# Kernel tuning notes

Measured on AMD Instinct MI355X. Metric: run time of the kernel, lower is better.

Reference implementation:

```python
import jax, jax.numpy as jnp
import numpy as np

N_NODES = 100000
N_EDGES = 1600000
NIN = 128
NHID = 128
N_GRAPHS = 1024


def _gcn_conv(x, src, dst, norm, W, b, n_nodes):
    """PyG-style GCNConv: linear (no bias) -> normalized scatter-add -> + bias."""
    xw = x @ W                                   # [N, out]
    msg = xw[src] * norm[:, None]                # gather + edge-normalize, [E', out]
    out = jax.ops.segment_sum(msg, dst, num_segments=n_nodes)
    return out + b


def _gcn_norm(edge_index, n_nodes):
    """Add self-loops and compute symmetric deg^{-1/2} normalization per edge."""
    loops = jnp.arange(n_nodes, dtype=edge_index.dtype)
    src = jnp.concatenate([edge_index[0], loops])
    dst = jnp.concatenate([edge_index[1], loops])
    deg = jax.ops.segment_sum(jnp.ones_like(dst, dtype=jnp.float32), dst,
                              num_segments=n_nodes)
    deg_isqrt = jnp.where(deg > 0, jax.lax.rsqrt(jnp.maximum(deg, 1.0)), 0.0)
    norm = deg_isqrt[src] * deg_isqrt[dst]
    return src, dst, norm


def setup_inputs() -> dict:
    key = jax.random.key(0)
    ks = jax.random.split(key, 8)
    x = jax.random.normal(ks[0], (N_NODES, NIN), dtype=jnp.float32)
    edge_index = jax.random.randint(ks[1], (2, N_EDGES), 0, N_NODES, dtype=jnp.int64)
    batch = jnp.sort(jax.random.randint(ks[2], (N_NODES,), 0, N_GRAPHS, dtype=jnp.int64))
    s_in = 1.0 / np.sqrt(NIN)
    s_h = 1.0 / np.sqrt(NHID)
    return {
        "x": x,
        "edge_index": edge_index,
        "batch": batch,
        "W1": jax.random.normal(ks[3], (NIN, NHID), dtype=jnp.float32) * s_in,
        "b1": jnp.zeros((NHID,), dtype=jnp.float32),
        "W2": jax.random.normal(ks[4], (NHID, NHID), dtype=jnp.float32) * s_h,
        "b2": jnp.zeros((NHID,), dtype=jnp.float32),
        "W3": jax.random.normal(ks[5], (NHID, NHID), dtype=jnp.float32) * s_h,
        "b3": jnp.zeros((NHID,), dtype=jnp.float32),
        "Wfc": jax.random.normal(ks[6], (NHID, 1), dtype=jnp.float32) * s_h,
        "bfc": jnp.zeros((1,), dtype=jnp.float32),
    }


def reference(x, edge_index, batch, W1, b1, W2, b2, W3, b3, Wfc, bfc):
    n_nodes = x.shape[0]
    src, dst, norm = _gcn_norm(edge_index, n_nodes)
    h = jax.nn.relu(_gcn_conv(x, src, dst, norm, W1, b1, n_nodes))
    h = jax.nn.relu(_gcn_conv(h, src, dst, norm, W2, b2, n_nodes))
    h = jax.nn.relu(_gcn_conv(h, src, dst, norm, W3, b3, n_nodes))
    # global mean pool over graphs in the batch
    sums = jax.ops.segment_sum(h, batch, num_segments=N_GRAPHS)      # [G, NHID]
    cnts = jax.ops.segment_sum(jnp.ones((n_nodes,), dtype=h.dtype), batch,
                               num_segments=N_GRAPHS)
    pooled = sums / jnp.maximum(cnts, 1.0)[:, None]
    return pooled @ Wfc + bfc                                        # [G, 1]
```

## Files before the change

### kernel.cpp

```cpp
#include <hip/hip_runtime.h>

#define N_NODES   100000
#define N_EDGES   1600000
#define NFEAT     128
#define N_GRAPHS  1024

#define BSHIFT  8
#define BNODES  256
#define NBUCK   391
#define BCAP    4608
#define SC_EDGES 4096
#define SC_EPT   8
#define SC_BLOCKS 391
#define BD_EPT   18

#define WT_STRIDE 136
#define GEMM_BLOCKS 782

typedef unsigned int uint32;
typedef unsigned short ushort;
typedef __attribute__((ext_vector_type(8))) short short8;
typedef __attribute__((ext_vector_type(4))) float f32x4;

__device__ inline ushort f2b(float f) {
    uint32 x = __float_as_uint(f);
    uint32 r = x + 0x7fffu + ((x >> 16) & 1u);
    return (ushort)(r >> 16);
}
__device__ inline float blo(uint32 u) { return __uint_as_float(u << 16); }
__device__ inline float bhi(uint32 u) { return __uint_as_float(u & 0xffff0000u); }

__device__ inline short8 cvt8(const float* p) {
    float4 v0 = ((const float4*)p)[0];
    float4 v1 = ((const float4*)p)[1];
    short8 r;
    r[0] = (short)f2b(v0.x); r[1] = (short)f2b(v0.y);
    r[2] = (short)f2b(v0.z); r[3] = (short)f2b(v0.w);
    r[4] = (short)f2b(v1.x); r[5] = (short)f2b(v1.y);
    r[6] = (short)f2b(v1.z); r[7] = (short)f2b(v1.w);
    return r;
}

__global__ __launch_bounds__(256) void k_castw(const float* __restrict__ W1, const float* __restrict__ W2,
                                               const float* __restrict__ W3, ushort* __restrict__ WT,
                                               int* __restrict__ cur) {
    int i = blockIdx.x * blockDim.x + threadIdx.x;
    if (i < NBUCK) cur[i] = 0;
    if (i >= 3 * NFEAT * NFEAT) return;
    int l = i >> 14;
    int j = i & 16383;
    int n = j >> 7;
    int k = j & 127;
    const float* W = (l == 0) ? W1 : (l == 1) ? W2 : W3;
    WT[i] = f2b(W[k * NFEAT + n]);
}

struct SMemScatter {
    int hist[NBUCK], lofs[NBUCK], gbase[NBUCK];
    int wsum[4];
    uint32 sortedP[SC_EDGES];
    ushort sortedB[SC_EDGES];
};

__global__ __launch_bounds__(512) void k_phase1(const int* __restrict__ src, const int* __restrict__ dst,
                                                int* __restrict__ cur, uint32* __restrict__ bbuf,
                                                const float* __restrict__ A, const ushort* __restrict__ WTl,
                                                ushort* __restrict__ C, int M) {
    __shared__ __align__(16) char smem[NFEAT * WT_STRIDE * 2];
    int t = threadIdx.x;
    if (blockIdx.x < SC_BLOCKS) {
        SMemScatter& S = *(SMemScatter*)smem;
        int e0 = blockIdx.x * SC_EDGES;
        int total = N_EDGES - e0; if (total > SC_EDGES) total = SC_EDGES; if (total < 0) total = 0;
        for (int i = t; i < NBUCK; i += 512) S.hist[i] = 0;
        __syncthreads();
        uint32 val[SC_EPT];
        int    meta[SC_EPT];
        #pragma unroll
        for (int k = 0; k < SC_EPT; ++k) {
            int i = t + k * 512;
            meta[k] = -1;
            if (i < total) {
                int s = src[e0 + i], d = dst[e0 + i];
                int b = d >> BSHIFT;
                int tk = atomicAdd(&S.hist[b], 1);
                val[k] = ((uint32)(d & (BNODES - 1)) << 17) | (uint32)s;
                meta[k] = (b << 13) | tk;
            }
        }
        __syncthreads();
        int inc = 0, ts = 0, h0 = 0;
        if (t < 256) {
            int b0 = 2 * t, b1 = 2 * t + 1;
            h0 = (b0 < NBUCK) ? S.hist[b0] : 0;
            int h1 = (b1 < NBUCK) ? S.hist[b1] : 0;
            ts = h0 + h1;
            int lane = t & 63;
            inc = ts;
            #pragma unroll
            for (int d = 1; d < 64; d <<= 1) {
                int u = __shfl_up(inc, d, 64);
                if (lane >= d) inc += u;
            }
            if (lane == 63) S.wsum[t >> 6] = inc;
        }
        __syncthreads();
        if (t < 256) {
            int w = t >> 6;
            int wpre = 0;
            for (int i = 0; i < w; ++i) wpre += S.wsum[i];
            int run = wpre + inc - ts;
            int b0 = 2 * t, b1 = 2 * t + 1;
            int h1 = ts - h0;
            if (b0 < NBUCK) {
                S.lofs[b0] = run;
                if (h0) S.gbase[b0] = atomicAdd(&cur[b0], h0);
            }
            if (b1 < NBUCK) {
                S.lofs[b1] = run + h0;
                if (h1) S.gbase[b1] = atomicAdd(&cur[b1], h1);
            }
        }
        __syncthreads();
        #pragma unroll
        for (int k = 0; k < SC_EPT; ++k) {
            if (meta[k] >= 0) {
                int b = meta[k] >> 13;
                int p = S.lofs[b] + (meta[k] & 0x1FFF);
                S.sortedP[p] = val[k];
                S.sortedB[p] = (ushort)b;
            }
        }
        __syncthreads();
        for (int i = t; i < total; i += 512) {
            int b = S.sortedB[i];
            int addr = S.gbase[b] + (i - S.lofs[b]);
            if (addr < BCAP)
                bbuf[(size_t)b * BCAP + addr] = S.sortedP[i];
        }
    } else {
        ushort* sWT = (ushort*)smem;
        int gb = blockIdx.x - SC_BLOCKS;
        for (int i = t; i < NFEAT * 16; i += 512) {
            int n = i >> 4, c = i & 15;
            *(float4*)(sWT + n * WT_STRIDE + c * 8) = ((const float4*)WTl)[i];
        }
        int wave = t >> 6, lane = t & 63;
        int m0 = gb * 128 + wave * 16;
        int mRow = m0 + (lane & 15);
        if (mRow >= M) mRow = M - 1;
        int kg = lane >> 4;
        const float* Ap = A + (size_t)mRow * NFEAT + kg * 8;
        short8 a0 = cvt8(Ap);
        short8 a1 = cvt8(Ap + 32);
        short8 a2 = cvt8(Ap + 64);
        short8 a3 = cvt8(Ap + 96);
        __syncthreads();

        f32x4 acc[8];
        #pragma unroll
        for (int nt = 0; nt < 8; ++nt) acc[nt] = (f32x4){0.f, 0.f, 0.f, 0.f};
        #pragma unroll
        for (int nt = 0; nt < 8; ++nt) {
            int n = nt * 16 + (lane & 15);
            const short8* Bp = (const short8*)(sWT + n * WT_STRIDE + kg * 8);
            short8 b0 = Bp[0];
            short8 b1 = Bp[4];
            short8 b2 = Bp[8];
            short8 b3 = Bp[12];
            acc[nt] = __builtin_amdgcn_mfma_f32_16x16x32_bf16(a0, b0, acc[nt], 0, 0, 0);
            acc[nt] = __builtin_amdgcn_mfma_f32_16x16x32_bf16(a1, b1, acc[nt], 0, 0, 0);
            acc[nt] = __builtin_amdgcn_mfma_f32_16x16x32_bf16(a2, b2, acc[nt], 0, 0, 0);
            acc[nt] = __builtin_amdgcn_mfma_f32_16x16x32_bf16(a3, b3, acc[nt], 0, 0, 0);
        }
        __syncthreads();
        {
            int colBase = lane & 15;
            #pragma unroll
            for (int r = 0; r < 4; ++r) {
                int lr = wave * 16 + kg * 4 + r;
                #pragma unroll
                for (int nt = 0; nt < 8; ++nt)
                    sWT[lr * NFEAT + nt * 16 + colBase] = f2b(acc[nt][r]);
            }
        }
        __syncthreads();
        {
            int rowBase = gb * 128;
            const float4* sC4 = (const float4*)sWT;
            for (int i = t; i < 2048; i += 512) {
                int row = i >> 4;
                int gr = rowBase + row;
                if (gr < M) ((float4*)(C + (size_t)gr * NFEAT))[i & 15] = sC4[i];
            }
        }
    }
}

__global__ __launch_bounds__(256) void k_build(const uint32* __restrict__ bbuf, const int* __restrict__ cur,
                                               int* __restrict__ col, int* __restrict__ offsets,
                                               float* __restrict__ dinv) {
    int b = blockIdx.x;
    __shared__ int hist[BNODES], excl[BNODES];
    __shared__ int wsum[4], wtot[4];
    __shared__ int sorted[BCAP];
    __shared__ int sBase, sTotal;
    int t = threadIdx.x;
    {
        int pre = 0, tot = 0;
        #pragma unroll
        for (int q = 0; q < 2; ++q) {
            int i = 2 * t + q;
            if (i < NBUCK) {
                int v = cur[i]; if (v > BCAP) v = BCAP;
                tot += v;
                if (i < b) pre += v;
            }
        }
        int lane = t & 63, w = t >> 6;
        #pragma unroll
        for (int d = 32; d > 0; d >>= 1) { pre += __shfl_down(pre, d, 64); tot += __shfl_down(tot, d, 64); }
        if (lane == 0) { wsum[w] = pre; wtot[w] = tot; }
        __syncthreads();
        if (t == 0) {
            sBase = wsum[0] + wsum[1] + wsum[2] + wsum[3];
            sTotal = wtot[0] + wtot[1] + wtot[2] + wtot[3];
        }
        hist[t] = 0;
    }
    __syncthreads();
    int base = sBase;
    if (b == NBUCK - 1 && t == 0) offsets[N_NODES] = sTotal;
    int cnt = cur[b]; if (cnt > BCAP) cnt = BCAP;
    const uint32* reg = bbuf + (size_t)b * BCAP;

    uint32 val[BD_EPT];
    int    meta[BD_EPT];
    #pragma unroll
    for (int k = 0; k < BD_EPT; ++k) {
        int i = t + k * 256;
        meta[k] = -1;
        if (i < cnt) {
            uint32 p = reg[i];
            int node = p >> 17;
            int tk = atomicAdd(&hist[node], 1);
            val[k] = p & 0x1FFFF;
            meta[k] = (node << 16) | tk;
        }
    }
    __syncthreads();
    {
        int c = hist[t];
        int lane = t & 63, w = t >> 6;
        int inc = c;
        #pragma unroll
        for (int d = 1; d < 64; d <<= 1) {
            int u = __shfl_up(inc, d, 64);
            if (lane >= d) inc += u;
        }
        if (lane == 63) wsum[w] = inc;
        __syncthreads();
        int wpre = 0;
        for (int i = 0; i < w; ++i) wpre += wsum[i];
        int e = wpre + inc - c;
        excl[t] = e;
        int node = (b << BSHIFT) + t;
        if (node < N_NODES) {
            offsets[node] = base + e;
            dinv[node] = rsqrtf((float)(c + 1));
        }
    }
    __syncthreads();
    #pragma unroll
    for (int k = 0; k < BD_EPT; ++k) {
        if (meta[k] >= 0) {
            int node = meta[k] >> 16;
            sorted[excl[node] + (meta[k] & 0xFFFF)] = (int)val[k];
        }
    }
    __syncthreads();
    for (int i = t; i < cnt; i += 256) col[base + i] = sorted[i];
}

__global__ __launch_bounds__(512) void k_gemm(const ushort* __restrict__ A,
                                              const ushort* __restrict__ WTl,
                                              ushort* __restrict__ C, int M) {
    __shared__ ushort sWT[NFEAT * WT_STRIDE];
    int t = threadIdx.x;
    for (int i = t; i < NFEAT * 16; i += 512) {
        int n = i >> 4, c = i & 15;
        *(float4*)(sWT + n * WT_STRIDE + c * 8) = ((const float4*)WTl)[i];
    }
    int wave = t >> 6, lane = t & 63;
    int m0 = blockIdx.x * 128 + wave * 16;
    int mRow = m0 + (lane & 15);
    if (mRow >= M) mRow = M - 1;
    int kg = lane >> 4;
    const short8* Ap = (const short8*)(A + (size_t)mRow * NFEAT + kg * 8);
    short8 a0 = Ap[0];
    short8 a1 = Ap[4];
    short8 a2 = Ap[8];
    short8 a3 = Ap[12];
    __syncthreads();

    f32x4 acc[8];
    #pragma unroll
    for (int nt = 0; nt < 8; ++nt) acc[nt] = (f32x4){0.f, 0.f, 0.f, 0.f};
    #pragma unroll
    for (int nt = 0; nt < 8; ++nt) {
        int n = nt * 16 + (lane & 15);
        const short8* Bp = (const short8*)(sWT + n * WT_STRIDE + kg * 8);
        short8 b0 = Bp[0];
        short8 b1 = Bp[4];
        short8 b2 = Bp[8];
        short8 b3 = Bp[12];
        acc[nt] = __builtin_amdgcn_mfma_f32_16x16x32_bf16(a0, b0, acc[nt], 0, 0, 0);
        acc[nt] = __builtin_amdgcn_mfma_f32_16x16x32_bf16(a1, b1, acc[nt], 0, 0, 0);
        acc[nt] = __builtin_amdgcn_mfma_f32_16x16x32_bf16(a2, b2, acc[nt], 0, 0, 0);
        acc[nt] = __builtin_amdgcn_mfma_f32_16x16x32_bf16(a3, b3, acc[nt], 0, 0, 0);
    }
    __syncthreads();
    {
        int colBase = lane & 15;
        #pragma unroll
        for (int r = 0; r < 4; ++r) {
            int lr = wave * 16 + kg * 4 + r;
            #pragma unroll
            for (int nt = 0; nt < 8; ++nt)
                sWT[lr * NFEAT + nt * 16 + colBase] = f2b(acc[nt][r]);
        }
    }
    __syncthreads();
    {
        int rowBase = blockIdx.x * 128;
        const float4* sC4 = (const float4*)sWT;
        for (int i = t; i < 2048; i += 512) {
            int row = i >> 4;
            int gr = rowBase + row;
            if (gr < M) ((float4*)(C + (size_t)gr * NFEAT))[i & 15] = sC4[i];
        }
    }
}

#define AGG_BODY4 \
    float dn = dinv[n]; \
    int half = lane >> 4; \
    int fl = lane & 15; \
    const uint4* XW4 = (const uint4*)XWu; \
    uint4 sv = XW4[(size_t)n * 16 + fl]; \
    float ws = (half == 0) ? dn * dn : 0.f; \
    float a0 = ws * blo(sv.x), a1 = ws * bhi(sv.x); \
    float a2 = ws * blo(sv.y), a3 = ws * bhi(sv.y); \
    float a4 = ws * blo(sv.z), a5 = ws * bhi(sv.z); \
    float a6 = ws * blo(sv.w), a7 = ws * bhi(sv.w); \
    int e0 = off[n], e1 = off[n + 1]; \
    for (int base = e0; base < e1; base += 64) { \
        int len = e1 - base; if (len > 64) len = 64; \
        int cm = (lane < len) ? col[base + lane] : 0; \
        float wm = (lane < len) ? dn * dinv[cm] : 0.f; \
        int j = 0; \
        for (; j + 16 <= len; j += 16) { \
            uint4 u[4]; float w[4]; \
            _Pragma("unroll") \
            for (int p = 0; p < 4; ++p) { \
                int idx = j + 4 * p + half; \
                int cc = __shfl(cm, idx, 64); \
                w[p] = __shfl(wm, idx, 64); \
                u[p] = XW4[(size_t)cc * 16 + fl]; \
            } \
            _Pragma("unroll") \
            for (int p = 0; p < 4; ++p) { \
                a0 = fmaf(w[p], blo(u[p].x), a0); a1 = fmaf(w[p], bhi(u[p].x), a1); \
                a2 = fmaf(w[p], blo(u[p].y), a2); a3 = fmaf(w[p], bhi(u[p].y), a3); \
                a4 = fmaf(w[p], blo(u[p].z), a4); a5 = fmaf(w[p], bhi(u[p].z), a5); \
                a6 = fmaf(w[p], blo(u[p].w), a6); a7 = fmaf(w[p], bhi(u[p].w), a7); \
            } \
        } \
        for (; j < len; j += 4) { \
            int rem = len - j; \
            int idx = j + ((half < rem) ? half : 0); \
            int cc = __shfl(cm, idx, 64); \
            float ww = __shfl(wm, idx, 64); \
            if (half >= rem) ww = 0.f; \
            uint4 u = XW4[(size_t)cc * 16 + fl]; \
            a0 = fmaf(ww, blo(u.x), a0); a1 = fmaf(ww, bhi(u.x), a1); \
            a2 = fmaf(ww, blo(u.y), a2); a3 = fmaf(ww, bhi(u.y), a3); \
            a4 = fmaf(ww, blo(u.z), a4); a5 = fmaf(ww, bhi(u.z), a5); \
            a6 = fmaf(ww, blo(u.w), a6); a7 = fmaf(ww, bhi(u.w), a7); \
        } \
    } \
    a0 += __shfl_xor(a0, 32, 64); a0 += __shfl_xor(a0, 16, 64); \
    a1 += __shfl_xor(a1, 32, 64); a1 += __shfl_xor(a1, 16, 64); \
    a2 += __shfl_xor(a2, 32, 64); a2 += __shfl_xor(a2, 16, 64); \
    a3 += __shfl_xor(a3, 32, 64); a3 += __shfl_xor(a3, 16, 64); \
    a4 += __shfl_xor(a4, 32, 64); a4 += __shfl_xor(a4, 16, 64); \
    a5 += __shfl_xor(a5, 32, 64); a5 += __shfl_xor(a5, 16, 64); \
    a6 += __shfl_xor(a6, 32, 64); a6 += __shfl_xor(a6, 16, 64); \
    a7 += __shfl_xor(a7, 32, 64); a7 += __shfl_xor(a7, 16, 64);

__global__ __launch_bounds__(256) void k_agg(const uint32* __restrict__ XWu, const int* __restrict__ col,
                                             const int* __restrict__ off, const float* __restrict__ dinv,
                                             const float* __restrict__ bias, uint32* __restrict__ Hu) {
    int wid = (blockIdx.x * blockDim.x + threadIdx.x) >> 6;
    int lane = threadIdx.x & 63;
    if (wid >= N_NODES) return;
    int n = wid;
    AGG_BODY4
    if (half == 0) {
        float4 bb0 = ((const float4*)bias)[2 * fl];
        float4 bb1 = ((const float4*)bias)[2 * fl + 1];
        float r0 = fmaxf(a0 + bb0.x, 0.f), r1 = fmaxf(a1 + bb0.y, 0.f);
        float r2 = fmaxf(a2 + bb0.z, 0.f), r3 = fmaxf(a3 + bb0.w, 0.f);
        float r4 = fmaxf(a4 + bb1.x, 0.f), r5 = fmaxf(a5 + bb1.y, 0.f);
        float r6 = fmaxf(a6 + bb1.z, 0.f), r7 = fmaxf(a7 + bb1.w, 0.f);
        uint4 o;
        o.x = (uint32)f2b(r0) | ((uint32)f2b(r1) << 16);
        o.y = (uint32)f2b(r2) | ((uint32)f2b(r3) << 16);
        o.z = (uint32)f2b(r4) | ((uint32)f2b(r5) << 16);
        o.w = (uint32)f2b(r6) | ((uint32)f2b(r7) << 16);
        ((uint4*)Hu)[(size_t)n * 16 + fl] = o;
    }
}

__global__ __launch_bounds__(256) void k_agg_fc(const uint32* __restrict__ XWu, const int* __restrict__ col,
                                                const int* __restrict__ off, const float* __restrict__ dinv,
                                                const float* __restrict__ bias, const float* __restrict__ Wfc,
                                                float* __restrict__ nodeS) {
    int wid = (blockIdx.x * blockDim.x + threadIdx.x) >> 6;
    int lane = threadIdx.x & 63;
    if (wid >= N_NODES) return;
    int n = wid;
    AGG_BODY4
    float4 bb0 = ((const float4*)bias)[2 * fl];
    float4 bb1 = ((const float4*)bias)[2 * fl + 1];
    float4 wf0 = ((const float4*)Wfc)[2 * fl];
    float4 wf1 = ((const float4*)Wfc)[2 * fl + 1];
    float s = fmaxf(a0 + bb0.x, 0.f) * wf0.x + fmaxf(a1 + bb0.y, 0.f) * wf0.y
            + fmaxf(a2 + bb0.z, 0.f) * wf0.z + fmaxf(a3 + bb0.w, 0.f) * wf0.w
            + fmaxf(a4 + bb1.x, 0.f) * wf1.x + fmaxf(a5 + bb1.y, 0.f) * wf1.y
            + fmaxf(a6 + bb1.z, 0.f) * wf1.z + fmaxf(a7 + bb1.w, 0.f) * wf1.w;
    s += __shfl_xor(s, 8, 64);
    s += __shfl_xor(s, 4, 64);
    s += __shfl_xor(s, 2, 64);
    s += __shfl_xor(s, 1, 64);
    if (lane == 0) nodeS[n] = s;
}

__device__ inline int lower_bound_dev(const int* a, int n, int key) {
    int lo = 0, hi = n;
    while (lo < hi) {
        int mid = (lo + hi) >> 1;
        if (a[mid] < key) lo = mid + 1; else hi = mid;
    }
    return lo;
}

__global__ __launch_bounds__(256) void k_pool(const float* __restrict__ nodeS, const int* __restrict__ batch,
                                              const float* __restrict__ bfc, float* __restrict__ out) {
    int g = blockIdx.x;
    int t = threadIdx.x;
    int lo = lower_bound_dev(batch, N_NODES, g);
    int hi = lower_bound_dev(batch, N_NODES, g + 1);
    float s = 0.f;
    for (int i = lo + t; i < hi; i += 256) s += nodeS[i];
    for (int d = 32; d > 0; d >>= 1) s += __shfl_down(s, d, 64);
    __shared__ float ws[4];
    int lane = t & 63, w = t >> 6;
    if (lane == 0) ws[w] = s;
    __syncthreads();
    if (t == 0) {
        float tot = ws[0] + ws[1] + ws[2] + ws[3];
        float cnt = (float)(hi - lo);
        out[g] = tot / fmaxf(cnt, 1.0f) + bfc[0];
    }
}

extern "C" void kernel_launch(void* const* d_in, const int* in_sizes, int n_in,
                              void* d_out, int out_size, void* d_ws, size_t ws_size,
                              hipStream_t stream) {
    const float* x    = (const float*)d_in[0];
    const int*   ei   = (const int*)d_in[1];
    const int*   batch= (const int*)d_in[2];
    const float* W1   = (const float*)d_in[3];
    const float* b1   = (const float*)d_in[4];
    const float* W2   = (const float*)d_in[5];
    const float* b2   = (const float*)d_in[6];
    const float* W3   = (const float*)d_in[7];
    const float* b3   = (const float*)d_in[8];
    const float* Wfc  = (const float*)d_in[9];
    const float* bfc  = (const float*)d_in[10];
    float* out = (float*)d_out;

    const int* src = ei;
    const int* dst = ei + N_EDGES;

    char* p = (char*)d_ws;
    auto carve = [&](size_t bytes) { void* r = (void*)p; p += (bytes + 255) & ~(size_t)255; return r; };
    int*    cur       = (int*)   carve(sizeof(int) * NBUCK);
    uint32* bbuf      = (uint32*)carve(sizeof(uint32) * (size_t)NBUCK * BCAP);
    float*  dinv      = (float*) carve(sizeof(float) * N_NODES);
    int*    offsets   = (int*)   carve(sizeof(int) * (N_NODES + 1));
    int*    col       = (int*)   carve(sizeof(int) * N_EDGES);
    ushort* XW        = (ushort*)carve(sizeof(short) * (size_t)N_NODES * NFEAT);
    ushort* H         = (ushort*)carve(sizeof(short) * (size_t)N_NODES * NFEAT);
    ushort* WT        = (ushort*)carve(sizeof(short) * 3 * NFEAT * NFEAT);
    float*  nodeS     = (float*) carve(sizeof(float) * N_NODES);

    const int waveNodeBlocks = (N_NODES * 64 + 255) / 256;

    k_castw<<<(3 * NFEAT * NFEAT + 255) / 256, 256, 0, stream>>>(W1, W2, W3, WT, cur);
    k_phase1<<<SC_BLOCKS + GEMM_BLOCKS, 512, 0, stream>>>(src, dst, cur, bbuf, x, WT, XW, N_NODES);
    k_build<<<NBUCK, 256, 0, stream>>>(bbuf, cur, col, offsets, dinv);

    k_agg<<<waveNodeBlocks, 256, 0, stream>>>((const uint32*)XW, col, offsets, dinv, b1, (uint32*)H);
    k_gemm<<<GEMM_BLOCKS, 512, 0, stream>>>(H, WT + NFEAT * NFEAT, XW, N_NODES);
    k_agg<<<waveNodeBlocks, 256, 0, stream>>>((const uint32*)XW, col, offsets, dinv, b2, (uint32*)H);
    k_gemm<<<GEMM_BLOCKS, 512, 0, stream>>>(H, WT + 2 * NFEAT * NFEAT, XW, N_NODES);
    k_agg_fc<<<waveNodeBlocks, 256, 0, stream>>>((const uint32*)XW, col, offsets, dinv, b3, Wfc, nodeS);

    k_pool<<<N_GRAPHS, 256, 0, stream>>>(nodeS, batch, bfc, out);
}
```

Measured before the change: 372.5 us.

## Split first-layer GEMM across scatter and CSR-build kernels, drop weight cast kernel

Removes the standalone weight-cast kernel: W1 is converted and transposed straight into shared memory inside the GEMM body, and the W2/W3 casts run as extra blocks in phase 1. The first-layer X·W1 GEMM is split in half, one half co-scheduled with the edge scatter and the other half with the CSR build, which now uses 512 threads. The goal is to fill the GPU during the latency-bound graph-preprocessing kernels and cut one launch. The trade-off is that every GEMM block recasts W1 from fp32 with scattered 2-byte LDS writes, and the counter reset becomes a memset.

New measurement: 378.4 us. Within noise of the previous version (+1.6%).

```diff
diff --git a/kernel.cpp b/kernel.cpp
--- a/kernel.cpp
+++ b/kernel.cpp
@@ -12,10 +12,12 @@
 #define SC_EDGES 4096
 #define SC_EPT   8
 #define SC_BLOCKS 391
-#define BD_EPT   18
+#define CW_BLOCKS 64
+#define BD_EPT   9
 
 #define WT_STRIDE 136
 #define GEMM_BLOCKS 782
+#define GEMM_SPLIT  391
 
 typedef unsigned int uint32;
 typedef unsigned short ushort;
@@ -41,18 +43,67 @@
     return r;
 }
 
-__global__ __launch_bounds__(256) void k_castw(const float* __restrict__ W1, const float* __restrict__ W2,
-                                               const float* __restrict__ W3, ushort* __restrict__ WT,
-                                               int* __restrict__ cur) {
-    int i = blockIdx.x * blockDim.x + threadIdx.x;
-    if (i < NBUCK) cur[i] = 0;
-    if (i >= 3 * NFEAT * NFEAT) return;
-    int l = i >> 14;
-    int j = i & 16383;
-    int n = j >> 7;
-    int k = j & 127;
-    const float* W = (l == 0) ? W1 : (l == 1) ? W2 : W3;
-    WT[i] = f2b(W[k * NFEAT + n]);
+__device__ __forceinline__ void gemm_x_body(ushort* sWT, int t, int gb,
+                                            const float* __restrict__ A,
+                                            const float* __restrict__ W1,
+                                            ushort* __restrict__ C, int M) {
+    for (int i = t; i < NFEAT * 32; i += 512) {
+        int k = i >> 5, n0 = (i & 31) * 4;
+        float4 v = ((const float4*)W1)[i];
+        sWT[(n0 + 0) * WT_STRIDE + k] = f2b(v.x);
+        sWT[(n0 + 1) * WT_STRIDE + k] = f2b(v.y);
+        sWT[(n0 + 2) * WT_STRIDE + k] = f2b(v.z);
+        sWT[(n0 + 3) * WT_STRIDE + k] = f2b(v.w);
+    }
+    int wave = t >> 6, lane = t & 63;
+    int m0 = gb * 128 + wave * 16;
+    int mRow = m0 + (lane & 15);
+    if (mRow >= M) mRow = M - 1;
+    int kg = lane >> 4;
+    const float* Ap = A + (size_t)mRow * NFEAT + kg * 8;
+    short8 a0 = cvt8(Ap);
+    short8 a1 = cvt8(Ap + 32);
+    short8 a2 = cvt8(Ap + 64);
+    short8 a3 = cvt8(Ap + 96);
+    __syncthreads();
+
+    f32x4 acc[8];
+    #pragma unroll
+    for (int nt = 0; nt < 8; ++nt) acc[nt] = (f32x4){0.f, 0.f, 0.f, 0.f};
+    #pragma unroll
+    for (int nt = 0; nt < 8; ++nt) {
+        int n = nt * 16 + (lane & 15);
+        const short8* Bp = (const short8*)(sWT + n * WT_STRIDE + kg * 8);
+        short8 b0 = Bp[0];
+        short8 b1 = Bp[4];
+        short8 b2 = Bp[8];
+        short8 b3 = Bp[12];
+        acc[nt] = __builtin_amdgcn_mfma_f32_16x16x32_bf16(a0, b0, acc[nt], 0, 0, 0);
+        acc[nt] = __builtin_amdgcn_mfma_f32_16x16x32_bf16(a1, b1, acc[nt], 0, 0, 0);
+        acc[nt] = __builtin_amdgcn_mfma_f32_16x16x32_bf16(a2, b2, acc[nt], 0, 0, 0);
+        acc[nt] = __builtin_amdgcn_mfma_f32_16x16x32_bf16(a3, b3, acc[nt], 0, 0, 0);
+    }
+    __syncthreads();
+    {
+        int colBase = lane & 15;
+        #pragma unroll
+        for (int r = 0; r < 4; ++r) {
+            int lr = wave * 16 + kg * 4 + r;
+            #pragma unroll
+            for (int nt = 0; nt < 8; ++nt)
+                sWT[lr * NFEAT + nt * 16 + colBase] = f2b(acc[nt][r]);
+        }
+    }
+    __syncthreads();
+    {
+        int rowBase = gb * 128;
+        const float4* sC4 = (const float4*)sWT;
+        for (int i = t; i < 2048; i += 512) {
+            int row = i >> 4;
+            int gr = rowBase + row;
+            if (gr < M) ((float4*)(C + (size_t)gr * NFEAT))[i & 15] = sC4[i];
+        }
+    }
 }
 
 struct SMemScatter {
@@ -64,8 +115,9 @@
 
 __global__ __launch_bounds__(512) void k_phase1(const int* __restrict__ src, const int* __restrict__ dst,
                                                 int* __restrict__ cur, uint32* __restrict__ bbuf,
-                                                const float* __restrict__ A, const ushort* __restrict__ WTl,
-                                                ushort* __restrict__ C, int M) {
+                                                const float* __restrict__ A, const float* __restrict__ W1,
+                                                const float* __restrict__ W2, const float* __restrict__ W3,
+                                                ushort* __restrict__ WT, ushort* __restrict__ C, int M) {
     __shared__ __align__(16) char smem[NFEAT * WT_STRIDE * 2];
     int t = threadIdx.x;
     if (blockIdx.x < SC_BLOCKS) {
@@ -138,148 +190,114 @@
             if (addr < BCAP)
                 bbuf[(size_t)b * BCAP + addr] = S.sortedP[i];
         }
+    } else if (blockIdx.x < SC_BLOCKS + CW_BLOCKS) {
+        int i = (blockIdx.x - SC_BLOCKS) * 512 + t;
+        int l = i >> 14;
+        int j = i & 16383;
+        int n = j >> 7;
+        int k = j & 127;
+        const float* W = l ? W3 : W2;
+        WT[i] = f2b(W[k * NFEAT + n]);
     } else {
-        ushort* sWT = (ushort*)smem;
-        int gb = blockIdx.x - SC_BLOCKS;
-        for (int i = t; i < NFEAT * 16; i += 512) {
-            int n = i >> 4, c = i & 15;
-            *(float4*)(sWT + n * WT_STRIDE + c * 8) = ((const float4*)WTl)[i];
-        }
-        int wave = t >> 6, lane = t & 63;
-        int m0 = gb * 128 + wave * 16;
-        int mRow = m0 + (lane & 15);
-        if (mRow >= M) mRow = M - 1;
-        int kg = lane >> 4;
-        const float* Ap = A + (size_t)mRow * NFEAT + kg * 8;
-        short8 a0 = cvt8(Ap);
-        short8 a1 = cvt8(Ap + 32);
-        short8 a2 = cvt8(Ap + 64);
-        short8 a3 = cvt8(Ap + 96);
-        __syncthreads();
-
-        f32x4 acc[8];
+        int gb = blockIdx.x - (SC_BLOCKS + CW_BLOCKS);
+        gemm_x_body((ushort*)smem, t, gb, A, W1, C, M);
+    }
+}
+
+__global__ __launch_bounds__(512) void k_phase2(const uint32* __restrict__ bbuf, const int* __restrict__ cur,
+                                                int* __restrict__ col, int* __restrict__ offsets,
+                                                float* __restrict__ dinv,
+                                                const float* __restrict__ A, const float* __restrict__ W1,
+                                                ushort* __restrict__ C, int M) {
+    __shared__ __align__(16) char smem[NFEAT * WT_STRIDE * 2];
+    int t = threadIdx.x;
+    if (blockIdx.x < NBUCK) {
+        struct SB {
+            int hist[BNODES], excl[BNODES];
+            int wsum[8], wtot[8];
+            int sorted[BCAP];
+            int sBase, sTotal;
+        };
+        SB& S = *(SB*)smem;
+        int b = blockIdx.x;
+        {
+            int v = 0;
+            if (t < NBUCK) { v = cur[t]; if (v > BCAP) v = BCAP; }
+            int pre = (t < b) ? v : 0;
+            int tot = v;
+            int lane = t & 63, w = t >> 6;
+            #pragma unroll
+            for (int d = 32; d > 0; d >>= 1) { pre += __shfl_down(pre, d, 64); tot += __shfl_down(tot, d, 64); }
+            if (lane == 0) { S.wsum[w] = pre; S.wtot[w] = tot; }
+            if (t < BNODES) S.hist[t] = 0;
+        }
+        __syncthreads();
+        if (t == 0) {
+            int pb = 0, tb2 = 0;
+            #pragma unroll
+            for (int i = 0; i < 8; ++i) { pb += S.wsum[i]; tb2 += S.wtot[i]; }
+            S.sBase = pb; S.sTotal = tb2;
+        }
+        __syncthreads();
+        int base = S.sBase;
+        if (b == NBUCK - 1 && t == 0) offsets[N_NODES] = S.sTotal;
+        int cnt = cur[b]; if (cnt > BCAP) cnt = BCAP;
+        const uint32* reg = bbuf + (size_t)b * BCAP;
+
+        uint32 val[BD_EPT];
+        int    meta[BD_EPT];
         #pragma unroll
-        for (int nt = 0; nt < 8; ++nt) acc[nt] = (f32x4){0.f, 0.f, 0.f, 0.f};
+        for (int k = 0; k < BD_EPT; ++k) {
+            int i = t + k * 512;
+            meta[k] = -1;
+            if (i < cnt) {
+                uint32 p = reg[i];
+                int node = p >> 17;
+                int tk = atomicAdd(&S.hist[node], 1);
+                val[k] = p & 0x1FFFF;
+                meta[k] = (node << 16) | tk;
+            }
+        }
+        __syncthreads();
+        int c = 0, inc = 0;
+        if (t < 256) {
+            c = S.hist[t];
+            int lane = t & 63;
+            inc = c;
+            #pragma unroll
+            for (int d = 1; d < 64; d <<= 1) {
+                int u = __shfl_up(inc, d, 64);
+                if (lane >= d) inc += u;
+            }
+            if (lane == 63) S.wsum[t >> 6] = inc;
+        }
+        __syncthreads();
+        if (t < 256) {
+            int w = t >> 6;
+            int wpre = 0;
+            for (int i = 0; i < w; ++i) wpre += S.wsum[i];
+            int e = wpre + inc - c;
+            S.excl[t] = e;
+            int node = (b << BSHIFT) + t;
+            if (node < N_NODES) {
+                offsets[node] = base + e;
+                dinv[node] = rsqrtf((float)(c + 1));
+            }
+        }
+        __syncthreads();
         #pragma unroll
-        for (int nt = 0; nt < 8; ++nt) {
-            int n = nt * 16 + (lane & 15);
-            const short8* Bp = (const short8*)(sWT + n * WT_STRIDE + kg * 8);
-            short8 b0 = Bp[0];
-            short8 b1 = Bp[4];
-            short8 b2 = Bp[8];
-            short8 b3 = Bp[12];
-            acc[nt] = __builtin_amdgcn_mfma_f32_16x16x32_bf16(a0, b0, acc[nt], 0, 0, 0);
-            acc[nt] = __builtin_amdgcn_mfma_f32_16x16x32_bf16(a1, b1, acc[nt], 0, 0, 0);
-            acc[nt] = __builtin_amdgcn_mfma_f32_16x16x32_bf16(a2, b2, acc[nt], 0, 0, 0);
-            acc[nt] = __builtin_amdgcn_mfma_f32_16x16x32_bf16(a3, b3, acc[nt], 0, 0, 0);
-        }
-        __syncthreads();
-        {
-            int colBase = lane & 15;
-            #pragma unroll
-            for (int r = 0; r < 4; ++r) {
-                int lr = wave * 16 + kg * 4 + r;
-                #pragma unroll
-                for (int nt = 0; nt < 8; ++nt)
-                    sWT[lr * NFEAT + nt * 16 + colBase] = f2b(acc[nt][r]);
-            }
-        }
-        __syncthreads();
-        {
-            int rowBase = gb * 128;
-            const float4* sC4 = (const float4*)sWT;
-            for (int i = t; i < 2048; i += 512) {
-                int row = i >> 4;
-                int gr = rowBase + row;
-                if (gr < M) ((float4*)(C + (size_t)gr * NFEAT))[i & 15] = sC4[i];
-            }
-        }
-    }
-}
-
-__global__ __launch_bounds__(256) void k_build(const uint32* __restrict__ bbuf, const int* __restrict__ cur,
-                                               int* __restrict__ col, int* __restrict__ offsets,
-                                               float* __restrict__ dinv) {
-    int b = blockIdx.x;
-    __shared__ int hist[BNODES], excl[BNODES];
-    __shared__ int wsum[4], wtot[4];
-    __shared__ int sorted[BCAP];
-    __shared__ int sBase, sTotal;
-    int t = threadIdx.x;
-    {
-        int pre = 0, tot = 0;
-        #pragma unroll
-        for (int q = 0; q < 2; ++q) {
-            int i = 2 * t + q;
-            if (i < NBUCK) {
-                int v = cur[i]; if (v > BCAP) v = BCAP;
-                tot += v;
-                if (i < b) pre += v;
-            }
-        }
-        int lane = t & 63, w = t >> 6;
-        #pragma unroll
-        for (int d = 32; d > 0; d >>= 1) { pre += __shfl_down(pre, d, 64); tot += __shfl_down(tot, d, 64); }
-        if (lane == 0) { wsum[w] = pre; wtot[w] = tot; }
-        __syncthreads();
-        if (t == 0) {
-            sBase = wsum[0] + wsum[1] + wsum[2] + wsum[3];
-            sTotal = wtot[0] + wtot[1] + wtot[2] + wtot[3];
-        }
-        hist[t] = 0;
-    }
-    __syncthreads();
-    int base = sBase;
-    if (b == NBUCK - 1 && t == 0) offsets[N_NODES] = sTotal;
-    int cnt = cur[b]; if (cnt > BCAP) cnt = BCAP;
-    const uint32* reg = bbuf + (size_t)b * BCAP;
-
-    uint32 val[BD_EPT];
-    int    meta[BD_EPT];
-    #pragma unroll
-    for (int k = 0; k < BD_EPT; ++k) {
-        int i = t + k * 256;
-        meta[k] = -1;
-        if (i < cnt) {
-            uint32 p = reg[i];
-            int node = p >> 17;
-            int tk = atomicAdd(&hist[node], 1);
-            val[k] = p & 0x1FFFF;
-            meta[k] = (node << 16) | tk;
-        }
-    }
-    __syncthreads();
-    {
-        int c = hist[t];
-        int lane = t & 63, w = t >> 6;
-        int inc = c;
-        #pragma unroll
-        for (int d = 1; d < 64; d <<= 1) {
-            int u = __shfl_up(inc, d, 64);
-            if (lane >= d) inc += u;
-        }
-        if (lane == 63) wsum[w] = inc;
-        __syncthreads();
-        int wpre = 0;
-        for (int i = 0; i < w; ++i) wpre += wsum[i];
-        int e = wpre + inc - c;
-        excl[t] = e;
-        int node = (b << BSHIFT) + t;
-        if (node < N_NODES) {
-            offsets[node] = base + e;
-            dinv[node] = rsqrtf((float)(c + 1));
-        }
-    }
-    __syncthreads();
-    #pragma unroll
-    for (int k = 0; k < BD_EPT; ++k) {
-        if (meta[k] >= 0) {
-            int node = meta[k] >> 16;
-            sorted[excl[node] + (meta[k] & 0xFFFF)] = (int)val[k];
-        }
-    }
-    __syncthreads();
-    for (int i = t; i < cnt; i += 256) col[base + i] = sorted[i];
+        for (int k = 0; k < BD_EPT; ++k) {
+            if (meta[k] >= 0) {
+                int node = meta[k] >> 16;
+                S.sorted[S.excl[node] + (meta[k] & 0xFFFF)] = (int)val[k];
+            }
+        }
+        __syncthreads();
+        for (int i = t; i < cnt; i += 512) col[base + i] = S.sorted[i];
+    } else {
+        int gb = blockIdx.x;
+        gemm_x_body((ushort*)smem, t, gb, A, W1, C, M);
+    }
 }
 
 __global__ __launch_bounds__(512) void k_gemm(const ushort* __restrict__ A,
@@ -503,19 +521,21 @@
     int*    col       = (int*)   carve(sizeof(int) * N_EDGES);
     ushort* XW        = (ushort*)carve(sizeof(short) * (size_t)N_NODES * NFEAT);
     ushort* H         = (ushort*)carve(sizeof(short) * (size_t)N_NODES * NFEAT);
-    ushort* WT        = (ushort*)carve(sizeof(short) * 3 * NFEAT * NFEAT);
+    ushort* WT        = (ushort*)carve(sizeof(short) * 2 * NFEAT * NFEAT);
     float*  nodeS     = (float*) carve(sizeof(float) * N_NODES);
 
     const int waveNodeBlocks = (N_NODES * 64 + 255) / 256;
 
-    k_castw<<<(3 * NFEAT * NFEAT + 255) / 256, 256, 0, stream>>>(W1, W2, W3, WT, cur);
-    k_phase1<<<SC_BLOCKS + GEMM_BLOCKS, 512, 0, stream>>>(src, dst, cur, bbuf, x, WT, XW, N_NODES);
-    k_build<<<NBUCK, 256, 0, stream>>>(bbuf, cur, col, offsets, dinv);
+    hipMemsetAsync(cur, 0, sizeof(int) * NBUCK, stream);
+    k_phase1<<<SC_BLOCKS + CW_BLOCKS + GEMM_SPLIT, 512, 0, stream>>>(
+        src, dst, cur, bbuf, x, W1, W2, W3, WT, XW, N_NODES);
+    k_phase2<<<NBUCK + (GEMM_BLOCKS - GEMM_SPLIT), 512, 0, stream>>>(
+        bbuf, cur, col, offsets, dinv, x, W1, XW, N_NODES);
 
     k_agg<<<waveNodeBlocks, 256, 0, stream>>>((const uint32*)XW, col, offsets, dinv, b1, (uint32*)H);
+    k_gemm<<<GEMM_BLOCKS, 512, 0, stream>>>(H, WT, XW, N_NODES);
+    k_agg<<<waveNodeBlocks, 256, 0, stream>>>((const uint32*)XW, col, offsets, dinv, b2, (uint32*)H);
     k_gemm<<<GEMM_BLOCKS, 512, 0, stream>>>(H, WT + NFEAT * NFEAT, XW, N_NODES);
-    k_agg<<<waveNodeBlocks, 256, 0, stream>>>((const uint32*)XW, col, offsets, dinv, b2, (uint32*)H);
-    k_gemm<<<GEMM_BLOCKS, 512, 0, stream>>>(H, WT + 2 * NFEAT * NFEAT, XW, N_NODES);
     k_agg_fc<<<waveNodeBlocks, 256, 0, stream>>>((const uint32*)XW, col, offsets, dinv, b3, Wfc, nodeS);
 
     k_pool<<<N_GRAPHS, 256, 0, stream>>>(nodeS, batch, bfc, out);
```
